# Kernel tuning notes

Hardware: AMD Instinct MI355X
Metric: run time of the kernel (lower is better)

The kernel has to match this reference:

```python
import jax, jax.numpy as jnp
import numpy as np

EMBED_DIM = 1024
NUM_HEADS = 16
HEAD_DIM = EMBED_DIM // NUM_HEADS


def setup_inputs() -> dict:
    key = jax.random.key(0)
    ks = jax.random.split(key, 5)
    B, S, D = 2, 2048, EMBED_DIM
    scale = 1.0 / np.sqrt(D)
    x = jax.random.normal(ks[0], (B, S, D), dtype=jnp.float32)
    W_qkv = jax.random.normal(ks[1], (D, 3 * D), dtype=jnp.float32) * scale
    b_qkv = jnp.zeros((3 * D,), dtype=jnp.float32)
    W_out = jax.random.normal(ks[2], (D, D), dtype=jnp.float32) * scale
    b_out = jnp.zeros((D,), dtype=jnp.float32)
    return {"x": x, "W_qkv": W_qkv, "b_qkv": b_qkv, "W_out": W_out, "b_out": b_out}


def reference(x, W_qkv, b_qkv, W_out, b_out):
    B, S, D = x.shape
    H, Hd = NUM_HEADS, HEAD_DIM
    qkv = x @ W_qkv + b_qkv                       # [B,S,3D]
    qkv = qkv.reshape(B, S, 3, H, Hd)
    q = qkv[:, :, 0].transpose(0, 2, 1, 3)        # [B,H,S,Hd]
    k = qkv[:, :, 1].transpose(0, 2, 1, 3)
    v = qkv[:, :, 2].transpose(0, 2, 1, 3)
    scores = jnp.einsum('bhqd,bhkd->bhqk', q, k) / np.sqrt(Hd)  # [B,H,S,S]
    causal = jnp.tril(jnp.ones((S, S), dtype=bool))
    scores = jnp.where(causal[None, None], scores, -jnp.inf)
    attn = jax.nn.softmax(scores, axis=-1)
    out = jnp.einsum('bhqk,bhkd->bhqd', attn, v)  # [B,H,S,Hd]
    out = out.transpose(0, 2, 1, 3).reshape(B, S, D)
    return out @ W_out + b_out
```

## Files before the change

### kernel.cpp

```cpp
#include <hip/hip_runtime.h>
#include <hip/hip_bf16.h>
#include <math.h>

#define EMBED_DIM 1024
#define NUM_HEADS 16
#define HEAD_DIM 64
#define BATCH 2
#define SEQ 2048

using short8  = __attribute__((ext_vector_type(8))) short;
using floatx4 = __attribute__((ext_vector_type(4))) float;

__device__ __forceinline__ ushort f2bf(float f) {
    unsigned u = __float_as_uint(f);
    u = (u + 0x7FFFu + ((u >> 16) & 1u)) >> 16;
    return (ushort)u;
}

__device__ __forceinline__ unsigned bfpack2(float a, float b) {
    return ((__float_as_uint(a) + 0x8000u) >> 16) |
           (((__float_as_uint(b) + 0x8000u) >> 16) << 16);
}

__device__ __forceinline__ void load_lds16(const ushort* g, ushort* l) {
    __builtin_amdgcn_global_load_lds(
        (const __attribute__((address_space(1))) void*)g,
        (__attribute__((address_space(3))) void*)l, 16, 0, 0);
}

__device__ __forceinline__ void tc_tile(
    const float* __restrict__ W, ushort* __restrict__ Wt,
    int K, int N, int n0, int k0, float (*t)[65])
{
    const int c = threadIdx.x & 63, r0 = (threadIdx.x >> 6) * 16;
    #pragma unroll
    for (int r = 0; r < 16; ++r)
        t[r0 + r][c] = W[(size_t)(k0 + r0 + r) * N + n0 + c];
    __syncthreads();
    #pragma unroll
    for (int r = 0; r < 16; ++r)
        Wt[(size_t)(n0 + r0 + r) * K + k0 + c] = f2bf(t[c][r0 + r]);
}

__global__ __launch_bounds__(256) void prep_all(
    const float* __restrict__ x, const float* __restrict__ W_qkv,
    const float* __restrict__ W_out,
    ushort* __restrict__ xb, ushort* __restrict__ Wqb_t, ushort* __restrict__ Wob_t)
{
    __shared__ float t[64][65];
    const int bx = blockIdx.x;
    if (bx < 4096) {
        int i = (bx * 256 + threadIdx.x) * 4;
        float4 v = *(const float4*)&x[i];
        ushort4 o = { f2bf(v.x), f2bf(v.y), f2bf(v.z), f2bf(v.w) };
        *(ushort4*)&xb[i] = o;
    } else if (bx < 4096 + 768) {
        int b = bx - 4096;
        tc_tile(W_qkv, Wqb_t, 1024, 3072, (b % 48) * 64, (b / 48) * 64, t);
    } else {
        int b = bx - 4864;
        tc_tile(W_out, Wob_t, 1024, 1024, (b % 16) * 64, (b / 16) * 64, t);
    }
}

#define GK 1024

__device__ __forceinline__ void gemm_core(
    const ushort* __restrict__ A, const ushort* __restrict__ Bt,
    int m0, int n0, ushort* As0, ushort* As1, ushort* Bs0, ushort* Bs1,
    floatx4 acc[4][4])
{
    const int tid  = threadIdx.x;
    const int w    = tid >> 6;
    const int lane = tid & 63;
    const int col  = lane & 15;
    const int quad = lane >> 4;
    const int wm   = w >> 1, wn = w & 1;

    #pragma unroll
    for (int i = 0; i < 4; ++i)
        #pragma unroll
        for (int j = 0; j < 4; ++j)
            acc[i][j] = (floatx4){0.f, 0.f, 0.f, 0.f};

    const int o0   = w * 2048 + lane * 16;
    const int row0 = o0 >> 6;
    const int ke0  = (o0 & 63) >> 1;
    const int loff = (w * 2048) >> 1;

    const ushort* ga = A  + (size_t)(m0 + row0) * GK + ke0;
    const ushort* gb = Bt + (size_t)(n0 + row0) * GK + ke0;

    #pragma unroll
    for (int t = 0; t < 2; ++t) {
        load_lds16(ga + (size_t)t * 16 * GK, As0 + loff + t * 512);
        load_lds16(gb + (size_t)t * 16 * GK, Bs0 + loff + t * 512);
    }
    __syncthreads();

    for (int k0 = 0; k0 < GK; k0 += 32) {
        const int cur = (k0 >> 5) & 1;
        ushort* Ac = cur ? As1 : As0;
        ushort* Bc = cur ? Bs1 : Bs0;
        ushort* An = cur ? As0 : As1;
        ushort* Bn = cur ? Bs0 : Bs1;

        if (k0 + 32 < GK) {
            #pragma unroll
            for (int t = 0; t < 2; ++t) {
                load_lds16(ga + (k0 + 32) + (size_t)t * 16 * GK, An + loff + t * 512);
                load_lds16(gb + (k0 + 32) + (size_t)t * 16 * GK, Bn + loff + t * 512);
            }
        }

        short8 af[4], bf[4];
        #pragma unroll
        for (int i = 0; i < 4; ++i)
            af[i] = *(const short8*)&Ac[(wm * 64 + i * 16 + col) * 32 + quad * 8];
        #pragma unroll
        for (int j = 0; j < 4; ++j)
            bf[j] = *(const short8*)&Bc[(wn * 64 + j * 16 + col) * 32 + quad * 8];
        #pragma unroll
        for (int i = 0; i < 4; ++i)
            #pragma unroll
            for (int j = 0; j < 4; ++j)
                acc[i][j] = __builtin_amdgcn_mfma_f32_16x16x32_bf16(af[i], bf[j], acc[i][j], 0, 0, 0);

        __syncthreads();
    }
}

__global__ __launch_bounds__(256) void gemm_qkv_mfma(
    const ushort* __restrict__ A, const ushort* __restrict__ Bt,
    const float* __restrict__ bias,
    ushort* __restrict__ Qb, ushort* __restrict__ Kb, ushort* __restrict__ Vt)
{
    __shared__ __align__(16) ushort As[2][128 * 32];
    __shared__ __align__(16) ushort Bs[2][128 * 32];
    const int n0 = blockIdx.x * 128;
    const int m0 = blockIdx.y * 128;

    floatx4 acc[4][4];
    gemm_core(A, Bt, m0, n0, As[0], As[1], Bs[0], Bs[1], acc);

    const int lane = threadIdx.x & 63;
    const int w    = threadIdx.x >> 6;
    const int col  = lane & 15, quad = lane >> 4;
    const int wm   = w >> 1, wn = w & 1;

    #pragma unroll
    for (int j = 0; j < 4; ++j) {
        const int n = n0 + wn * 64 + j * 16 + col;
        const float bj = bias[n];
        const int part = n >> 10;
        const int h = (n >> 6) & 15;
        const int d = n & 63;
        #pragma unroll
        for (int i = 0; i < 4; ++i)
            #pragma unroll
            for (int r = 0; r < 4; ++r) {
                const int m = m0 + wm * 64 + i * 16 + quad * 4 + r;
                const int b = m >> 11, s = m & 2047;
                const int bh = b * 16 + h;
                const ushort bv = f2bf(acc[i][j][r] + bj);
                if (part == 0)      Qb[((size_t)bh * SEQ + s) * 64 + d] = bv;
                else if (part == 1) Kb[((size_t)bh * SEQ + s) * 64 + d] = bv;
                else                Vt[((size_t)bh * 64 + d) * SEQ + s] = bv;
            }
    }
}

__global__ __launch_bounds__(256) void gemm_out_mfma(
    const ushort* __restrict__ A, const ushort* __restrict__ Bt,
    const float* __restrict__ bias, float* __restrict__ out)
{
    __shared__ __align__(16) ushort As[2][128 * 32];
    __shared__ __align__(16) ushort Bs[2][128 * 32];
    const int n0 = blockIdx.x * 128;
    const int m0 = blockIdx.y * 128;

    floatx4 acc[4][4];
    gemm_core(A, Bt, m0, n0, As[0], As[1], Bs[0], Bs[1], acc);

    const int lane = threadIdx.x & 63;
    const int w    = threadIdx.x >> 6;
    const int col  = lane & 15, quad = lane >> 4;
    const int wm   = w >> 1, wn = w & 1;

    #pragma unroll
    for (int j = 0; j < 4; ++j) {
        const int n = n0 + wn * 64 + j * 16 + col;
        const float bj = bias[n];
        #pragma unroll
        for (int i = 0; i < 4; ++i)
            #pragma unroll
            for (int r = 0; r < 4; ++r) {
                const int m = m0 + wm * 64 + i * 16 + quad * 4 + r;
                out[(size_t)m * EMBED_DIM + n] = acc[i][j][r] + bj;
            }
    }
}

#define LP 72

__global__ __launch_bounds__(256) void attn_fused(
    const ushort* __restrict__ Qb, const ushort* __restrict__ Kb,
    const ushort* __restrict__ Vt, ushort* __restrict__ out)
{
    const int id = blockIdx.x;
    const int qt = 31 - (id >> 5);
    const int bh = id & 31;
    const int b  = bh >> 4, h = bh & 15;
    const int q0 = qt * 64;

    __shared__ __align__(16) ushort Qs[8 * 512];
    __shared__ __align__(16) ushort Ks[2][8 * 512];
    __shared__ __align__(16) ushort Vs[2][8 * 512];
    __shared__ __align__(16) ushort Ps[64 * LP];
    __shared__ __align__(16) float  ls[4][16];

    const int tid  = threadIdx.x;
    const int w    = tid >> 6;
    const int lane = tid & 63;
    const int col  = lane & 15;
    const int quad = lane >> 4;

    const ushort* kg[2];
    const ushort* vg[2];
    #pragma unroll
    for (int t = 0; t < 2; ++t) {
        kg[t] = Kb + (size_t)bh * SEQ * 64 + (size_t)(w * 16 + col) * 64 + t * 32 + quad * 8;
        vg[t] = Vt + (size_t)bh * 64 * SEQ + (size_t)(w * 16 + col) * SEQ + t * 32 + quad * 8;
    }

    {
        const ushort* Qg = Qb + ((size_t)bh * SEQ + q0) * 64;
        #pragma unroll
        for (int t = 0; t < 2; ++t) {
            load_lds16(Qg + (size_t)(w * 16 + col) * 64 + t * 32 + quad * 8,
                       &Qs[(w * 2 + t) * 512]);
            load_lds16(kg[t], &Ks[0][(w * 2 + t) * 512]);
            load_lds16(vg[t], &Vs[0][(w * 2 + t) * 512]);
            kg[t] += 64 * 64;
            vg[t] += 64;
        }
    }
    __syncthreads();

    const short8 a0 = *(const short8*)&Qs[(w * 2 + 0) * 512 + lane * 8];
    const short8 a1 = *(const short8*)&Qs[(w * 2 + 1) * 512 + lane * 8];

    floatx4 acc_o[4];
    #pragma unroll
    for (int dbi = 0; dbi < 4; ++dbi) acc_o[dbi] = (floatx4){0.f, 0.f, 0.f, 0.f};
    float l_lane = 0.f;
    const int myq = w * 16 + col;

    for (int kt = 0; kt <= qt; ++kt) {
        const int cur = kt & 1;
        const ushort* Kc = Ks[cur];
        const ushort* Vc = Vs[cur];

        if (kt < qt) {
            ushort* Kn = (ushort*)Ks[cur ^ 1];
            ushort* Vn = (ushort*)Vs[cur ^ 1];
            #pragma unroll
            for (int t = 0; t < 2; ++t) {
                load_lds16(kg[t], &Kn[(w * 2 + t) * 512]);
                load_lds16(vg[t], &Vn[(w * 2 + t) * 512]);
                kg[t] += 64 * 64;
                vg[t] += 64;
            }
        }

        floatx4 s_acc[4];
        #pragma unroll
        for (int kb = 0; kb < 4; ++kb) {
            short8 k0f = *(const short8*)&Kc[(kb * 2 + 0) * 512 + lane * 8];
            short8 k1f = *(const short8*)&Kc[(kb * 2 + 1) * 512 + lane * 8];
            floatx4 z = (floatx4){0.f, 0.f, 0.f, 0.f};
            z = __builtin_amdgcn_mfma_f32_16x16x32_bf16(k0f, a0, z, 0, 0, 0);
            z = __builtin_amdgcn_mfma_f32_16x16x32_bf16(k1f, a1, z, 0, 0, 0);
            s_acc[kb] = z;
        }

        if (kt == qt) {
            #pragma unroll
            for (int kb = 0; kb < 4; ++kb) {
                const int kbase = kb * 16 + quad * 4;
                float p[4];
                #pragma unroll
                for (int r = 0; r < 4; ++r) {
                    float e = __expf(s_acc[kb][r] * 0.125f);
                    p[r] = (kbase + r > myq) ? 0.f : e;
                    l_lane += p[r];
                }
                uint2 u = { bfpack2(p[0], p[1]), bfpack2(p[2], p[3]) };
                *(uint2*)&Ps[myq * LP + kbase] = u;
            }
        } else {
            #pragma unroll
            for (int kb = 0; kb < 4; ++kb) {
                const int kbase = kb * 16 + quad * 4;
                float p[4];
                #pragma unroll
                for (int r = 0; r < 4; ++r) {
                    p[r] = __expf(s_acc[kb][r] * 0.125f);
                    l_lane += p[r];
                }
                uint2 u = { bfpack2(p[0], p[1]), bfpack2(p[2], p[3]) };
                *(uint2*)&Ps[myq * LP + kbase] = u;
            }
        }

        short8 pa0 = *(const short8*)&Ps[(w * 16 + col) * LP + quad * 8];
        short8 pa1 = *(const short8*)&Ps[(w * 16 + col) * LP + 32 + quad * 8];
        #pragma unroll
        for (int dbi = 0; dbi < 4; ++dbi) {
            short8 vb0 = *(const short8*)&Vc[(dbi * 2 + 0) * 512 + lane * 8];
            short8 vb1 = *(const short8*)&Vc[(dbi * 2 + 1) * 512 + lane * 8];
            acc_o[dbi] = __builtin_amdgcn_mfma_f32_16x16x32_bf16(pa0, vb0, acc_o[dbi], 0, 0, 0);
            acc_o[dbi] = __builtin_amdgcn_mfma_f32_16x16x32_bf16(pa1, vb1, acc_o[dbi], 0, 0, 0);
        }

        __syncthreads();
    }

    l_lane += __shfl_xor(l_lane, 16);
    l_lane += __shfl_xor(l_lane, 32);
    if (quad == 0) ls[w][col] = 1.f / l_lane;
    float4 invv = *(const float4*)&ls[w][quad * 4];

    #pragma unroll
    for (int dbi = 0; dbi < 4; ++dbi)
        #pragma unroll
        for (int r = 0; r < 4; ++r) {
            int q = q0 + w * 16 + quad * 4 + r;
            int d = dbi * 16 + col;
            float inv = (r == 0) ? invv.x : (r == 1) ? invv.y : (r == 2) ? invv.z : invv.w;
            out[((size_t)(b * SEQ + q)) * EMBED_DIM + h * 64 + d] = f2bf(acc_o[dbi][r] * inv);
        }
}

extern "C" void kernel_launch(void* const* d_in, const int* in_sizes, int n_in,
                              void* d_out, int out_size, void* d_ws, size_t ws_size,
                              hipStream_t stream)
{
    const float* x     = (const float*)d_in[0];
    const float* W_qkv = (const float*)d_in[1];
    const float* b_qkv = (const float*)d_in[2];
    const float* W_out = (const float*)d_in[3];
    const float* b_out = (const float*)d_in[4];
    float* out = (float*)d_out;

    const int M  = BATCH * SEQ;
    const int D  = EMBED_DIM;
    const int N1 = 3 * D;
    const size_t HE = (size_t)BATCH * NUM_HEADS * SEQ * 64;

    ushort* xb    = (ushort*)d_ws;
    ushort* Wqb_t = xb + (size_t)M * D;
    ushort* Wob_t = Wqb_t + (size_t)D * N1;
    ushort* Qb    = Wob_t + (size_t)D * D;
    ushort* Kb    = Qb + HE;
    ushort* Vt    = Kb + HE;
    ushort* attnb = Vt + HE;

    prep_all<<<5120, 256, 0, stream>>>(x, W_qkv, W_out, xb, Wqb_t, Wob_t);

    gemm_qkv_mfma<<<dim3(N1 / 128, M / 128), 256, 0, stream>>>(
        xb, Wqb_t, b_qkv, Qb, Kb, Vt);

    attn_fused<<<dim3(32 * 32), 256, 0, stream>>>(Qb, Kb, Vt, attnb);

    gemm_out_mfma<<<dim3(D / 128, M / 128), 256, 0, stream>>>(
        attnb, Wob_t, b_out, out);
}
```

Baseline: 191.2 us.

## Enlarge attention query tile to 128 rows and restructure GEMM LDS layout

```diff
diff --git a/kernel.cpp b/kernel.cpp
--- a/kernel.cpp
+++ b/kernel.cpp
@@ -83,43 +83,44 @@
         for (int j = 0; j < 4; ++j)
             acc[i][j] = (floatx4){0.f, 0.f, 0.f, 0.f};
 
-    const int o0   = w * 2048 + lane * 16;
-    const int row0 = o0 >> 6;
-    const int ke0  = (o0 & 63) >> 1;
-    const int loff = (w * 2048) >> 1;
-
-    const ushort* ga = A  + (size_t)(m0 + row0) * GK + ke0;
-    const ushort* gb = Bt + (size_t)(n0 + row0) * GK + ke0;
-
+    const ushort* ga[2];
+    const ushort* gb[2];
     #pragma unroll
     for (int t = 0; t < 2; ++t) {
-        load_lds16(ga + (size_t)t * 16 * GK, As0 + loff + t * 512);
-        load_lds16(gb + (size_t)t * 16 * GK, Bs0 + loff + t * 512);
+        const int c = 2 * w + t;
+        ga[t] = A  + (size_t)(m0 + c * 16 + col) * GK + quad * 8;
+        gb[t] = Bt + (size_t)(n0 + c * 16 + col) * GK + quad * 8;
+    }
+
+    #pragma unroll
+    for (int t = 0; t < 2; ++t) {
+        load_lds16(ga[t], As0 + (2 * w + t) * 512);
+        load_lds16(gb[t], Bs0 + (2 * w + t) * 512);
     }
     __syncthreads();
 
     for (int k0 = 0; k0 < GK; k0 += 32) {
         const int cur = (k0 >> 5) & 1;
-        ushort* Ac = cur ? As1 : As0;
-        ushort* Bc = cur ? Bs1 : Bs0;
+        const ushort* Ac = cur ? As1 : As0;
+        const ushort* Bc = cur ? Bs1 : Bs0;
         ushort* An = cur ? As0 : As1;
         ushort* Bn = cur ? Bs0 : Bs1;
 
         if (k0 + 32 < GK) {
             #pragma unroll
             for (int t = 0; t < 2; ++t) {
-                load_lds16(ga + (k0 + 32) + (size_t)t * 16 * GK, An + loff + t * 512);
-                load_lds16(gb + (k0 + 32) + (size_t)t * 16 * GK, Bn + loff + t * 512);
+                load_lds16(ga[t] + k0 + 32, An + (2 * w + t) * 512);
+                load_lds16(gb[t] + k0 + 32, Bn + (2 * w + t) * 512);
             }
         }
 
         short8 af[4], bf[4];
         #pragma unroll
         for (int i = 0; i < 4; ++i)
-            af[i] = *(const short8*)&Ac[(wm * 64 + i * 16 + col) * 32 + quad * 8];
+            af[i] = *(const short8*)&Ac[(wm * 4 + i) * 512 + lane * 8];
         #pragma unroll
         for (int j = 0; j < 4; ++j)
-            bf[j] = *(const short8*)&Bc[(wn * 64 + j * 16 + col) * 32 + quad * 8];
+            bf[j] = *(const short8*)&Bc[(wn * 4 + j) * 512 + lane * 8];
         #pragma unroll
         for (int i = 0; i < 4; ++i)
             #pragma unroll
@@ -208,22 +209,31 @@
     const ushort* __restrict__ Vt, ushort* __restrict__ out)
 {
     const int id = blockIdx.x;
-    const int qt = 31 - (id >> 5);
+    const int qt = 15 - (id >> 5);
     const int bh = id & 31;
     const int b  = bh >> 4, h = bh & 15;
-    const int q0 = qt * 64;
-
-    __shared__ __align__(16) ushort Qs[8 * 512];
+    const int q0 = qt * 128;
+    const int nkt = qt * 2 + 2;
+
     __shared__ __align__(16) ushort Ks[2][8 * 512];
     __shared__ __align__(16) ushort Vs[2][8 * 512];
-    __shared__ __align__(16) ushort Ps[64 * LP];
-    __shared__ __align__(16) float  ls[4][16];
+    __shared__ __align__(16) ushort Ps[128 * LP];
+    __shared__ __align__(16) float  ls[4][2][16];
 
     const int tid  = threadIdx.x;
     const int w    = tid >> 6;
     const int lane = tid & 63;
     const int col  = lane & 15;
     const int quad = lane >> 4;
+    const int qbase = w * 32;
+
+    short8 qf[2][2];
+    #pragma unroll
+    for (int qg = 0; qg < 2; ++qg)
+        #pragma unroll
+        for (int kh = 0; kh < 2; ++kh)
+            qf[qg][kh] = *(const short8*)&Qb[((size_t)bh * SEQ + q0 + qbase + qg * 16 + col) * 64
+                                             + kh * 32 + quad * 8];
 
     const ushort* kg[2];
     const ushort* vg[2];
@@ -233,113 +243,130 @@
         vg[t] = Vt + (size_t)bh * 64 * SEQ + (size_t)(w * 16 + col) * SEQ + t * 32 + quad * 8;
     }
 
-    {
-        const ushort* Qg = Qb + ((size_t)bh * SEQ + q0) * 64;
-        #pragma unroll
-        for (int t = 0; t < 2; ++t) {
-            load_lds16(Qg + (size_t)(w * 16 + col) * 64 + t * 32 + quad * 8,
-                       &Qs[(w * 2 + t) * 512]);
-            load_lds16(kg[t], &Ks[0][(w * 2 + t) * 512]);
-            load_lds16(vg[t], &Vs[0][(w * 2 + t) * 512]);
-            kg[t] += 64 * 64;
-            vg[t] += 64;
-        }
+    #pragma unroll
+    for (int t = 0; t < 2; ++t) {
+        load_lds16(kg[t], &Ks[0][(2 * w + t) * 512]);
+        load_lds16(vg[t], &Vs[0][(2 * w + t) * 512]);
+        kg[t] += 64 * 64;
+        vg[t] += 64;
     }
     __syncthreads();
 
-    const short8 a0 = *(const short8*)&Qs[(w * 2 + 0) * 512 + lane * 8];
-    const short8 a1 = *(const short8*)&Qs[(w * 2 + 1) * 512 + lane * 8];
-
-    floatx4 acc_o[4];
-    #pragma unroll
-    for (int dbi = 0; dbi < 4; ++dbi) acc_o[dbi] = (floatx4){0.f, 0.f, 0.f, 0.f};
-    float l_lane = 0.f;
-    const int myq = w * 16 + col;
-
-    for (int kt = 0; kt <= qt; ++kt) {
+    floatx4 acc_o[4][2];
+    #pragma unroll
+    for (int dbi = 0; dbi < 4; ++dbi)
+        #pragma unroll
+        for (int qg = 0; qg < 2; ++qg)
+            acc_o[dbi][qg] = (floatx4){0.f, 0.f, 0.f, 0.f};
+    float l_lane[2] = {0.f, 0.f};
+
+    for (int kt = 0; kt < nkt; ++kt) {
         const int cur = kt & 1;
         const ushort* Kc = Ks[cur];
         const ushort* Vc = Vs[cur];
-
-        if (kt < qt) {
+        const int k0g = kt * 64;
+
+        if (kt + 1 < nkt) {
             ushort* Kn = (ushort*)Ks[cur ^ 1];
             ushort* Vn = (ushort*)Vs[cur ^ 1];
             #pragma unroll
             for (int t = 0; t < 2; ++t) {
-                load_lds16(kg[t], &Kn[(w * 2 + t) * 512]);
-                load_lds16(vg[t], &Vn[(w * 2 + t) * 512]);
+                load_lds16(kg[t], &Kn[(2 * w + t) * 512]);
+                load_lds16(vg[t], &Vn[(2 * w + t) * 512]);
                 kg[t] += 64 * 64;
                 vg[t] += 64;
             }
         }
 
-        floatx4 s_acc[4];
+        floatx4 st[4][2];
         #pragma unroll
         for (int kb = 0; kb < 4; ++kb) {
             short8 k0f = *(const short8*)&Kc[(kb * 2 + 0) * 512 + lane * 8];
             short8 k1f = *(const short8*)&Kc[(kb * 2 + 1) * 512 + lane * 8];
-            floatx4 z = (floatx4){0.f, 0.f, 0.f, 0.f};
-            z = __builtin_amdgcn_mfma_f32_16x16x32_bf16(k0f, a0, z, 0, 0, 0);
-            z = __builtin_amdgcn_mfma_f32_16x16x32_bf16(k1f, a1, z, 0, 0, 0);
-            s_acc[kb] = z;
+            #pragma unroll
+            for (int qg = 0; qg < 2; ++qg) {
+                floatx4 z = (floatx4){0.f, 0.f, 0.f, 0.f};
+                z = __builtin_amdgcn_mfma_f32_16x16x32_bf16(k0f, qf[qg][0], z, 0, 0, 0);
+                z = __builtin_amdgcn_mfma_f32_16x16x32_bf16(k1f, qf[qg][1], z, 0, 0, 0);
+                st[kb][qg] = z;
+            }
         }
 
-        if (kt == qt) {
-            #pragma unroll
-            for (int kb = 0; kb < 4; ++kb) {
-                const int kbase = kb * 16 + quad * 4;
-                float p[4];
+        #pragma unroll
+        for (int qg = 0; qg < 2; ++qg) {
+            const int qmin = q0 + qbase + qg * 16;
+            ushort* prow = &Ps[(qbase + qg * 16 + col) * LP];
+            if (k0g + 63 <= qmin) {
                 #pragma unroll
-                for (int r = 0; r < 4; ++r) {
-                    float e = __expf(s_acc[kb][r] * 0.125f);
-                    p[r] = (kbase + r > myq) ? 0.f : e;
-                    l_lane += p[r];
+                for (int kb = 0; kb < 4; ++kb) {
+                    float p[4];
+                    #pragma unroll
+                    for (int r = 0; r < 4; ++r) {
+                        p[r] = __expf(st[kb][qg][r] * 0.125f);
+                        l_lane[qg] += p[r];
+                    }
+                    uint2 u = { bfpack2(p[0], p[1]), bfpack2(p[2], p[3]) };
+                    *(uint2*)&prow[kb * 16 + quad * 4] = u;
                 }
-                uint2 u = { bfpack2(p[0], p[1]), bfpack2(p[2], p[3]) };
-                *(uint2*)&Ps[myq * LP + kbase] = u;
-            }
-        } else {
-            #pragma unroll
-            for (int kb = 0; kb < 4; ++kb) {
-                const int kbase = kb * 16 + quad * 4;
-                float p[4];
+            } else {
+                const int qg_g = qmin + col;
                 #pragma unroll
-                for (int r = 0; r < 4; ++r) {
-                    p[r] = __expf(s_acc[kb][r] * 0.125f);
-                    l_lane += p[r];
+                for (int kb = 0; kb < 4; ++kb) {
+                    const int kbase = k0g + kb * 16 + quad * 4;
+                    float p[4];
+                    #pragma unroll
+                    for (int r = 0; r < 4; ++r) {
+                        float e = __expf(st[kb][qg][r] * 0.125f);
+                        p[r] = (kbase + r > qg_g) ? 0.f : e;
+                        l_lane[qg] += p[r];
+                    }
+                    uint2 u = { bfpack2(p[0], p[1]), bfpack2(p[2], p[3]) };
+                    *(uint2*)&prow[kb * 16 + quad * 4] = u;
                 }
-                uint2 u = { bfpack2(p[0], p[1]), bfpack2(p[2], p[3]) };
-                *(uint2*)&Ps[myq * LP + kbase] = u;
             }
         }
 
-        short8 pa0 = *(const short8*)&Ps[(w * 16 + col) * LP + quad * 8];
-        short8 pa1 = *(const short8*)&Ps[(w * 16 + col) * LP + 32 + quad * 8];
+        short8 pa[2][2];
+        #pragma unroll
+        for (int qg = 0; qg < 2; ++qg)
+            #pragma unroll
+            for (int kh = 0; kh < 2; ++kh)
+                pa[qg][kh] = *(const short8*)&Ps[(qbase + qg * 16 + col) * LP + kh * 32 + quad * 8];
         #pragma unroll
         for (int dbi = 0; dbi < 4; ++dbi) {
             short8 vb0 = *(const short8*)&Vc[(dbi * 2 + 0) * 512 + lane * 8];
             short8 vb1 = *(const short8*)&Vc[(dbi * 2 + 1) * 512 + lane * 8];
-            acc_o[dbi] = __builtin_amdgcn_mfma_f32_16x16x32_bf16(pa0, vb0, acc_o[dbi], 0, 0, 0);
-            acc_o[dbi] = __builtin_amdgcn_mfma_f32_16x16x32_bf16(pa1, vb1, acc_o[dbi], 0, 0, 0);
+            #pragma unroll
+            for (int qg = 0; qg < 2; ++qg) {
+                acc_o[dbi][qg] = __builtin_amdgcn_mfma_f32_16x16x32_bf16(pa[qg][0], vb0, acc_o[dbi][qg], 0, 0, 0);
+                acc_o[dbi][qg] = __builtin_amdgcn_mfma_f32_16x16x32_bf16(pa[qg][1], vb1, acc_o[dbi][qg], 0, 0, 0);
+            }
         }
 
         __syncthreads();
     }
 
-    l_lane += __shfl_xor(l_lane, 16);
-    l_lane += __shfl_xor(l_lane, 32);
-    if (quad == 0) ls[w][col] = 1.f / l_lane;
-    float4 invv = *(const float4*)&ls[w][quad * 4];
-
-    #pragma unroll
-    for (int dbi = 0; dbi < 4; ++dbi)
-        #pragma unroll
-        for (int r = 0; r < 4; ++r) {
-            int q = q0 + w * 16 + quad * 4 + r;
-            int d = dbi * 16 + col;
-            float inv = (r == 0) ? invv.x : (r == 1) ? invv.y : (r == 2) ? invv.z : invv.w;
-            out[((size_t)(b * SEQ + q)) * EMBED_DIM + h * 64 + d] = f2bf(acc_o[dbi][r] * inv);
-        }
+    #pragma unroll
+    for (int qg = 0; qg < 2; ++qg) {
+        float lr = l_lane[qg];
+        lr += __shfl_xor(lr, 16);
+        lr += __shfl_xor(lr, 32);
+        if (quad == 0) ls[w][qg][col] = 1.f / lr;
+    }
+
+    #pragma unroll
+    for (int qg = 0; qg < 2; ++qg) {
+        float4 invv = *(const float4*)&ls[w][qg][quad * 4];
+        #pragma unroll
+        for (int dbi = 0; dbi < 4; ++dbi)
+            #pragma unroll
+            for (int r = 0; r < 4; ++r) {
+                int q = q0 + qbase + qg * 16 + quad * 4 + r;
+                int d = dbi * 16 + col;
+                float inv = (r == 0) ? invv.x : (r == 1) ? invv.y : (r == 2) ? invv.z : invv.w;
+                out[((size_t)(b * SEQ + q)) * EMBED_DIM + h * 64 + d] = f2bf(acc_o[dbi][qg][r] * inv);
+            }
+    }
 }
 
 extern "C" void kernel_launch(void* const* d_in, const int* in_sizes, int n_in,
@@ -371,7 +398,7 @@
     gemm_qkv_mfma<<<dim3(N1 / 128, M / 128), 256, 0, stream>>>(
         xb, Wqb_t, b_qkv, Qb, Kb, Vt);
 
-    attn_fused<<<dim3(32 * 32), 256, 0, stream>>>(Qb, Kb, Vt, attnb);
+    attn_fused<<<dim3(16 * 32), 256, 0, stream>>>(Qb, Kb, Vt, attnb);
 
     gemm_out_mfma<<<dim3(D / 128, M / 128), 256, 0, stream>>>(
         attnb, Wob_t, b_out, out);
```

Measured after the change: 232.9 us. 1.22x slower.

## Load Q fragments directly to registers and use per-wave fragment-layout P buffer

Applied to the files above, without the earlier changes.

```diff
diff --git a/kernel.cpp b/kernel.cpp
--- a/kernel.cpp
+++ b/kernel.cpp
@@ -201,8 +201,6 @@
     }
 }
 
-#define LP 72
-
 __global__ __launch_bounds__(256) void attn_fused(
     const ushort* __restrict__ Qb, const ushort* __restrict__ Kb,
     const ushort* __restrict__ Vt, ushort* __restrict__ out)
@@ -213,11 +211,9 @@
     const int b  = bh >> 4, h = bh & 15;
     const int q0 = qt * 64;
 
-    __shared__ __align__(16) ushort Qs[8 * 512];
     __shared__ __align__(16) ushort Ks[2][8 * 512];
     __shared__ __align__(16) ushort Vs[2][8 * 512];
-    __shared__ __align__(16) ushort Ps[64 * LP];
-    __shared__ __align__(16) float  ls[4][16];
+    __shared__ __align__(16) ushort Ps[4 * 1024];
 
     const int tid  = threadIdx.x;
     const int w    = tid >> 6;
@@ -225,6 +221,12 @@
     const int col  = lane & 15;
     const int quad = lane >> 4;
 
+    short8 qf[2];
+    #pragma unroll
+    for (int kh = 0; kh < 2; ++kh)
+        qf[kh] = *(const short8*)&Qb[((size_t)bh * SEQ + q0 + w * 16 + col) * 64
+                                     + kh * 32 + quad * 8];
+
     const ushort* kg[2];
     const ushort* vg[2];
     #pragma unroll
@@ -233,27 +235,22 @@
         vg[t] = Vt + (size_t)bh * 64 * SEQ + (size_t)(w * 16 + col) * SEQ + t * 32 + quad * 8;
     }
 
-    {
-        const ushort* Qg = Qb + ((size_t)bh * SEQ + q0) * 64;
-        #pragma unroll
-        for (int t = 0; t < 2; ++t) {
-            load_lds16(Qg + (size_t)(w * 16 + col) * 64 + t * 32 + quad * 8,
-                       &Qs[(w * 2 + t) * 512]);
-            load_lds16(kg[t], &Ks[0][(w * 2 + t) * 512]);
-            load_lds16(vg[t], &Vs[0][(w * 2 + t) * 512]);
-            kg[t] += 64 * 64;
-            vg[t] += 64;
-        }
+    #pragma unroll
+    for (int t = 0; t < 2; ++t) {
+        load_lds16(kg[t], &Ks[0][(2 * w + t) * 512]);
+        load_lds16(vg[t], &Vs[0][(2 * w + t) * 512]);
+        kg[t] += 64 * 64;
+        vg[t] += 64;
     }
     __syncthreads();
-
-    const short8 a0 = *(const short8*)&Qs[(w * 2 + 0) * 512 + lane * 8];
-    const short8 a1 = *(const short8*)&Qs[(w * 2 + 1) * 512 + lane * 8];
 
     floatx4 acc_o[4];
     #pragma unroll
     for (int dbi = 0; dbi < 4; ++dbi) acc_o[dbi] = (floatx4){0.f, 0.f, 0.f, 0.f};
     float l_lane = 0.f;
+
+    ushort* Pw = &Ps[w * 1024];
+    const int pq = (quad & 1) * 4;
     const int myq = w * 16 + col;
 
     for (int kt = 0; kt <= qt; ++kt) {
@@ -266,22 +263,22 @@
             ushort* Vn = (ushort*)Vs[cur ^ 1];
             #pragma unroll
             for (int t = 0; t < 2; ++t) {
-                load_lds16(kg[t], &Kn[(w * 2 + t) * 512]);
-                load_lds16(vg[t], &Vn[(w * 2 + t) * 512]);
+                load_lds16(kg[t], &Kn[(2 * w + t) * 512]);
+                load_lds16(vg[t], &Vn[(2 * w + t) * 512]);
                 kg[t] += 64 * 64;
                 vg[t] += 64;
             }
         }
 
-        floatx4 s_acc[4];
+        floatx4 st[4];
         #pragma unroll
         for (int kb = 0; kb < 4; ++kb) {
             short8 k0f = *(const short8*)&Kc[(kb * 2 + 0) * 512 + lane * 8];
             short8 k1f = *(const short8*)&Kc[(kb * 2 + 1) * 512 + lane * 8];
             floatx4 z = (floatx4){0.f, 0.f, 0.f, 0.f};
-            z = __builtin_amdgcn_mfma_f32_16x16x32_bf16(k0f, a0, z, 0, 0, 0);
-            z = __builtin_amdgcn_mfma_f32_16x16x32_bf16(k1f, a1, z, 0, 0, 0);
-            s_acc[kb] = z;
+            z = __builtin_amdgcn_mfma_f32_16x16x32_bf16(k0f, qf[0], z, 0, 0, 0);
+            z = __builtin_amdgcn_mfma_f32_16x16x32_bf16(k1f, qf[1], z, 0, 0, 0);
+            st[kb] = z;
         }
 
         if (kt == qt) {
@@ -291,30 +288,29 @@
                 float p[4];
                 #pragma unroll
                 for (int r = 0; r < 4; ++r) {
-                    float e = __expf(s_acc[kb][r] * 0.125f);
+                    float e = __expf(st[kb][r] * 0.125f);
                     p[r] = (kbase + r > myq) ? 0.f : e;
                     l_lane += p[r];
                 }
                 uint2 u = { bfpack2(p[0], p[1]), bfpack2(p[2], p[3]) };
-                *(uint2*)&Ps[myq * LP + kbase] = u;
+                *(uint2*)&Pw[(kb >> 1) * 512 + (col + 16 * ((kb & 1) * 2 + (quad >> 1))) * 8 + pq] = u;
             }
         } else {
             #pragma unroll
             for (int kb = 0; kb < 4; ++kb) {
-                const int kbase = kb * 16 + quad * 4;
                 float p[4];
                 #pragma unroll
                 for (int r = 0; r < 4; ++r) {
-                    p[r] = __expf(s_acc[kb][r] * 0.125f);
+                    p[r] = __expf(st[kb][r] * 0.125f);
                     l_lane += p[r];
                 }
                 uint2 u = { bfpack2(p[0], p[1]), bfpack2(p[2], p[3]) };
-                *(uint2*)&Ps[myq * LP + kbase] = u;
-            }
-        }
-
-        short8 pa0 = *(const short8*)&Ps[(w * 16 + col) * LP + quad * 8];
-        short8 pa1 = *(const short8*)&Ps[(w * 16 + col) * LP + 32 + quad * 8];
+                *(uint2*)&Pw[(kb >> 1) * 512 + (col + 16 * ((kb & 1) * 2 + (quad >> 1))) * 8 + pq] = u;
+            }
+        }
+
+        short8 pa0 = *(const short8*)&Pw[0 * 512 + lane * 8];
+        short8 pa1 = *(const short8*)&Pw[1 * 512 + lane * 8];
         #pragma unroll
         for (int dbi = 0; dbi < 4; ++dbi) {
             short8 vb0 = *(const short8*)&Vc[(dbi * 2 + 0) * 512 + lane * 8];
@@ -328,8 +324,13 @@
 
     l_lane += __shfl_xor(l_lane, 16);
     l_lane += __shfl_xor(l_lane, 32);
-    if (quad == 0) ls[w][col] = 1.f / l_lane;
-    float4 invv = *(const float4*)&ls[w][quad * 4];
+    const float inv = 1.f / l_lane;
+    float invq[4];
+    #pragma unroll
+    for (int r = 0; r < 4; ++r) {
+        int iv = __builtin_amdgcn_ds_bpermute((quad * 4 + r) << 2, __float_as_int(inv));
+        invq[r] = __int_as_float(iv);
+    }
 
     #pragma unroll
     for (int dbi = 0; dbi < 4; ++dbi)
@@ -337,8 +338,7 @@
         for (int r = 0; r < 4; ++r) {
             int q = q0 + w * 16 + quad * 4 + r;
             int d = dbi * 16 + col;
-            float inv = (r == 0) ? invv.x : (r == 1) ? invv.y : (r == 2) ? invv.z : invv.w;
-            out[((size_t)(b * SEQ + q)) * EMBED_DIM + h * 64 + d] = f2bf(acc_o[dbi][r] * inv);
+            out[((size_t)(b * SEQ + q)) * EMBED_DIM + h * 64 + d] = f2bf(acc_o[dbi][r] * invq[r]);
         }
 }
 
```

Result: slower. 196.5 us (+2.8%).
